# Performance work log

Measured on AMD Instinct MI355X. Metric: run time of the kernel, lower is better.

Reference implementation:

```python
import jax, jax.numpy as jnp
import numpy as np

NUM_USERS = 80000
NUM_ITEMS = 40000
NUM_NODES = NUM_USERS + NUM_ITEMS
LATENT_DIM = 64
N_LAYERS = 3
ALPHA = 0.8
E_POS = 3_000_000
E_NEG = 1_500_000
E_PATH = 2_000_000
N_PATHS = 6


def _make_edges(rng, n_edges, n_nodes):
    # sample keys, dedupe so COO is coalesced (distinct (row,col) pairs)
    keys = rng.integers(0, n_nodes * n_nodes, size=int(n_edges * 1.05), dtype=np.int64)
    keys = np.unique(keys)[:n_edges]
    assert keys.shape[0] == n_edges
    row = (keys // n_nodes).astype(np.int32)
    col = (keys % n_nodes).astype(np.int32)
    return row, col


def setup_inputs() -> dict:
    key = jax.random.key(0)
    k1, k2, k3, k4, k5 = jax.random.split(key, 5)
    rng = np.random.default_rng(0)

    pos_row, pos_col = _make_edges(rng, E_POS, NUM_NODES)
    neg_row, neg_col = _make_edges(rng, E_NEG, NUM_NODES)
    p_row, p_col = _make_edges(rng, E_PATH, NUM_NODES)

    # path membership counts: for each coalesced edge, how many times each of the
    # 6 path matrices contains it (0/1 here); at least one path per edge
    counts = (rng.random((E_PATH, N_PATHS)) < 0.5).astype(np.float32)
    empty = counts.sum(axis=1) == 0
    counts[empty, 0] = 1.0

    return {
        "user_emb": 0.1 * jax.random.normal(k1, (NUM_USERS, LATENT_DIM), jnp.float32),
        "item_emb": 0.1 * jax.random.normal(k2, (NUM_ITEMS, LATENT_DIM), jnp.float32),
        "theta": jnp.ones((N_PATHS,), jnp.float32) / N_PATHS,
        "pos_row": jnp.asarray(pos_row),
        "pos_col": jnp.asarray(pos_col),
        "pos_val": jax.random.uniform(k3, (E_POS,), jnp.float32, 0.01, 1.0),
        "neg_row": jnp.asarray(neg_row),
        "neg_col": jnp.asarray(neg_col),
        "neg_val": jax.random.uniform(k4, (E_NEG,), jnp.float32, 0.01, 1.0),
        "p_row": jnp.asarray(p_row),
        "p_col": jnp.asarray(p_col),
        "p_counts": jnp.asarray(counts),
    }


def _spmm(row, col, val, x, n_nodes):
    # y = A @ x with A given as COO edge list: gather + segment scatter-add
    return jax.ops.segment_sum(val[:, None] * x[col], row, num_segments=n_nodes)


def reference(user_emb, item_emb, theta, pos_row, pos_col, pos_val,
              neg_row, neg_col, neg_val, p_row, p_col, p_counts):
    n = NUM_NODES

    # ---- build path-weighted matrix (coalesce + sparse row softmax, eq.(2)) ----
    theta_w = jax.nn.softmax(theta)                 # [6]
    vals = p_counts @ theta_w                       # coalesced values per edge [E_path]
    exp_v = jnp.exp(vals)
    row_sums = jax.ops.segment_sum(exp_v, p_row, num_segments=n)
    soft_v = exp_v / (row_sums[p_row] + 1e-12)      # row-level sparse softmax

    # ---- PEE: E_0 = P @ all_emb ----
    all_emb = jnp.concatenate([user_emb, item_emb], axis=0)  # [N, D]
    e = _spmm(p_row, p_col, soft_v, all_emb, n)
    embs = [e]

    # ---- signed propagation ----
    for _ in range(N_LAYERS):
        e_pos = _spmm(pos_row, pos_col, pos_val, e, n)
        e_neg_a = _spmm(neg_row, neg_col, neg_val, e, n)
        e = e_pos + ALPHA * (e - e_neg_a)
        embs.append(e)

    light_out = jnp.mean(jnp.stack(embs, axis=1), axis=1)   # [N, D]
    users = light_out[:NUM_USERS]
    items = light_out[NUM_USERS:]
    return users, items
```

## Files before the change

### kernel.cpp

```cpp
#include <hip/hip_runtime.h>

#define NUM_USERS 80000
#define NUM_ITEMS 40000
#define NUM_NODES 120000
#define DIM 64
#define ALPHA_C 0.8f

typedef unsigned short u16;
typedef unsigned int u32;
typedef int   i2v __attribute__((ext_vector_type(2)));
typedef u32   u4v __attribute__((ext_vector_type(4)));
typedef float f4v __attribute__((ext_vector_type(4)));

__device__ __forceinline__ u16 f2bf(float f) {
    union { float f; u32 i; } v;
    v.f = f;
    u32 i = v.i;
    u32 r = (i + 0x7FFFu + ((i >> 16) & 1u)) >> 16;
    return (u16)r;
}
__device__ __forceinline__ float lo_bf(u32 u) { return __uint_as_float(u << 16); }
__device__ __forceinline__ float hi_bf(u32 u) { return __uint_as_float(u & 0xffff0000u); }

__device__ __forceinline__ void acc8(float* __restrict__ acc, float v, uint4 q) {
    const u32* p = (const u32*)&q;
#pragma unroll
    for (int k = 0; k < 4; ++k) {
        u32 u = p[k];
        acc[2 * k]     = fmaf(v, lo_bf(u), acc[2 * k]);
        acc[2 * k + 1] = fmaf(v, hi_bf(u), acc[2 * k + 1]);
    }
}

__device__ __forceinline__ uint4 ldrow(const u16* __restrict__ x, int c, int li) {
    return *((const uint4*)(x + (size_t)c * DIM) + li);
}

template <bool SUMV, bool PACKED>
__device__ __forceinline__ void seg_pipe(const int* __restrict__ cp0,
                                         const float* __restrict__ vp0,
                                         const i2v* __restrict__ ep0,
                                         int start, int end,
                                         const u16* __restrict__ x,
                                         int li,
                                         float* __restrict__ acc,
                                         float* __restrict__ vsum) {
    const int n = end - start;
    const int* cp = nullptr;
    const float* vp = nullptr;
    const i2v* ep = nullptr;
    if constexpr (PACKED) { ep = ep0 + start; }
    else { cp = cp0 + start; vp = vp0 + start; }

    auto LDE = [&](int i, int& c, float& v) {
        if constexpr (PACKED) {
            i2v e = ep[i];
            c = e.x;
            v = __int_as_float(e.y);
        } else {
            c = cp[i];
            v = vp[i];
        }
    };

    float s = 0.f;
    const int np = n >> 1;
    if (np >= 4) {
        int ca0, ca1, cb0, cb1, cc0, cc1, cd0, cd1;
        float va0, va1, vb0, vb1, vc0, vc1, vd0, vd1;
        LDE(0, ca0, va0); LDE(1, ca1, va1);
        LDE(2, cb0, vb0); LDE(3, cb1, vb1);
        LDE(4, cc0, vc0); LDE(5, cc1, vc1);
        LDE(6, cd0, vd0); LDE(7, cd1, vd1);
        uint4 xa0 = ldrow(x, ca0, li), xa1 = ldrow(x, ca1, li);
        uint4 xb0 = ldrow(x, cb0, li), xb1 = ldrow(x, cb1, li);
        for (int p = 4; p < np; ++p) {
            int ce0, ce1; float ve0, ve1;
            LDE(2 * p, ce0, ve0); LDE(2 * p + 1, ce1, ve1);
            uint4 xc0 = ldrow(x, cc0, li);
            uint4 xc1 = ldrow(x, cc1, li);
            acc8(acc, va0, xa0);
            acc8(acc, va1, xa1);
            if (SUMV) s += va0 + va1;
            va0 = vb0; va1 = vb1; vb0 = vc0; vb1 = vc1; vc0 = vd0; vc1 = vd1;
            vd0 = ve0; vd1 = ve1;
            cc0 = cd0; cc1 = cd1; cd0 = ce0; cd1 = ce1;
            xa0 = xb0; xa1 = xb1; xb0 = xc0; xb1 = xc1;
        }
        uint4 xc0 = ldrow(x, cc0, li), xc1 = ldrow(x, cc1, li);
        uint4 xd0 = ldrow(x, cd0, li), xd1 = ldrow(x, cd1, li);
        acc8(acc, va0, xa0); acc8(acc, va1, xa1);
        if (SUMV) s += va0 + va1;
        acc8(acc, vb0, xb0); acc8(acc, vb1, xb1);
        if (SUMV) s += vb0 + vb1;
        acc8(acc, vc0, xc0); acc8(acc, vc1, xc1);
        if (SUMV) s += vc0 + vc1;
        acc8(acc, vd0, xd0); acc8(acc, vd1, xd1);
        if (SUMV) s += vd0 + vd1;
        if (n & 1) {
            int c; float v;
            LDE(n - 1, c, v);
            uint4 xq = ldrow(x, c, li);
            acc8(acc, v, xq);
            if (SUMV) s += v;
        }
    } else {
        for (int e = 0; e < n; ++e) {
            int c; float v;
            LDE(e, c, v);
            uint4 xq = ldrow(x, c, li);
            acc8(acc, v, xq);
            if (SUMV) s += v;
        }
    }
    if (SUMV) *vsum = s;
}

__global__ void k_softmax_theta(const float* __restrict__ theta,
                                float* __restrict__ theta_w) {
    if (threadIdx.x == 0 && blockIdx.x == 0) {
        float m = -1e30f;
        for (int i = 0; i < 6; ++i) m = fmaxf(m, theta[i]);
        float e[6];
        float s = 0.f;
        for (int i = 0; i < 6; ++i) { e[i] = expf(theta[i] - m); s += e[i]; }
        for (int i = 0; i < 6; ++i) theta_w[i] = e[i] / s;
    }
}

__global__ void k_expv(const float* __restrict__ p_counts,
                       const float* __restrict__ theta_w,
                       float* __restrict__ exp_v, int E) {
    int i = blockIdx.x * blockDim.x + threadIdx.x;
    if (i >= E) return;
    const float* c = p_counts + (size_t)i * 6;
    float v = c[0] * theta_w[0] + c[1] * theta_w[1] + c[2] * theta_w[2] +
              c[3] * theta_w[3] + c[4] * theta_w[4] + c[5] * theta_w[5];
    exp_v[i] = expf(v);
}

__device__ __forceinline__ void lower_bound_ptr(const int* __restrict__ rows,
                                                int nnz, int r,
                                                int* __restrict__ ptr) {
    int lo = 0, hi = nnz;
    while (lo < hi) {
        int mid = (lo + hi) >> 1;
        if (rows[mid] < r) lo = mid + 1; else hi = mid;
    }
    ptr[r] = lo;
}

__global__ void k_row_ptr3(const int* __restrict__ rows_a, int nnz_a, int* __restrict__ pa,
                           const int* __restrict__ rows_b, int nnz_b, int* __restrict__ pb,
                           const int* __restrict__ rows_c, int nnz_c, int* __restrict__ pc) {
    int t = blockIdx.x * blockDim.x + threadIdx.x;
    int which = t / (NUM_NODES + 1);
    int r = t - which * (NUM_NODES + 1);
    if (which == 0) lower_bound_ptr(rows_a, nnz_a, r, pa);
    else if (which == 1) lower_bound_ptr(rows_b, nnz_b, r, pb);
    else if (which == 2) lower_bound_ptr(rows_c, nnz_c, r, pc);
}

__global__ void k_cvt(const float* __restrict__ user_emb,
                      const float* __restrict__ item_emb,
                      u16* __restrict__ emb16) {
    int i = blockIdx.x * blockDim.x + threadIdx.x;
    size_t f = (size_t)i * 4;
    const size_t UTOT = (size_t)NUM_USERS * DIM;
    const size_t TOT = (size_t)NUM_NODES * DIM;
    if (f >= TOT) return;
    float4 v = (f < UTOT) ? *(const float4*)(user_emb + f)
                          : *(const float4*)(item_emb + (f - UTOT));
    ushort4 o;
    o.x = f2bf(v.x); o.y = f2bf(v.y); o.z = f2bf(v.z); o.w = f2bf(v.w);
    *(ushort4*)(emb16 + f) = o;
}

__global__ void k_merge(const int* __restrict__ rp_p, const int* __restrict__ col_p,
                        const float* __restrict__ val_p,
                        const int* __restrict__ rp_n, const int* __restrict__ col_n,
                        const float* __restrict__ val_n,
                        i2v* __restrict__ mev, int* __restrict__ rp_m,
                        int nnz_total) {
    int t = blockIdx.x * blockDim.x + threadIdx.x;
    int row = t >> 3;
    if (row >= NUM_NODES) return;
    int li = threadIdx.x & 7;
    int sp = rp_p[row], np = rp_p[row + 1] - sp;
    int sn = rp_n[row], nn = rp_n[row + 1] - sn;
    int base = sp + sn;
    if (li == 0) {
        rp_m[row] = base;
        if (row == 0) rp_m[NUM_NODES] = nnz_total;
    }
    for (int i = li; i < np; i += 8) {
        i2v e;
        e.x = __builtin_nontemporal_load(col_p + sp + i);
        e.y = __float_as_int(__builtin_nontemporal_load(val_p + sp + i));
        __builtin_nontemporal_store(e, mev + base + i);
    }
    int b2 = base + np;
    for (int i = li; i < nn; i += 8) {
        i2v e;
        e.x = __builtin_nontemporal_load(col_n + sn + i);
        e.y = __float_as_int(-ALPHA_C * __builtin_nontemporal_load(val_n + sn + i));
        __builtin_nontemporal_store(e, mev + b2 + i);
    }
}

__global__ void k_path(const u16* __restrict__ emb16,
                       const float* __restrict__ exp_v,
                       const int* __restrict__ rp,
                       const int* __restrict__ cols,
                       u16* __restrict__ e0) {
    int t = blockIdx.x * blockDim.x + threadIdx.x;
    int row = t >> 3;
    if (row >= NUM_NODES) return;
    int li = threadIdx.x & 7;
    int start = rp[row], end = rp[row + 1];

    float acc[8];
#pragma unroll
    for (int k = 0; k < 8; ++k) acc[k] = 0.f;
    float s = 0.f;

    seg_pipe<true, false>(cols, exp_v, nullptr, start, end, emb16, li, acc, &s);

    float inv = 1.0f / (s + 1e-12f);
    u32 o[4];
#pragma unroll
    for (int k = 0; k < 4; ++k)
        o[k] = (u32)f2bf(acc[2 * k] * inv) | ((u32)f2bf(acc[2 * k + 1] * inv) << 16);
    u4v vv; vv.x = o[0]; vv.y = o[1]; vv.z = o[2]; vv.w = o[3];
    __builtin_nontemporal_store(vv, (u4v*)(e0 + (size_t)row * DIM) + li);
}

template <int FINAL>
__global__ void k_layer_t(const u16* __restrict__ e_in,
                          u16* __restrict__ e_out,
                          const u16* __restrict__ e0,
                          const u16* __restrict__ e1,
                          float* __restrict__ out,
                          const int* __restrict__ rp_m,
                          const i2v* __restrict__ mev) {
    int t = blockIdx.x * blockDim.x + threadIdx.x;
    int row = t >> 3;
    if (row >= NUM_NODES) return;
    int li = threadIdx.x & 7;

    float acc[8];
#pragma unroll
    for (int k = 0; k < 8; ++k) acc[k] = 0.f;

    seg_pipe<false, true>(nullptr, nullptr, mev, rp_m[row], rp_m[row + 1],
                          e_in, li, acc, nullptr);

    uint4 eq = *((const uint4*)(e_in + (size_t)row * DIM) + li);
    const u32* ep_ = (const u32*)&eq;
    float res[8];
#pragma unroll
    for (int k = 0; k < 4; ++k) {
        res[2 * k]     = acc[2 * k]     + ALPHA_C * lo_bf(ep_[k]);
        res[2 * k + 1] = acc[2 * k + 1] + ALPHA_C * hi_bf(ep_[k]);
    }

    if (FINAL) {
        u4v q0 = __builtin_nontemporal_load((const u4v*)(e0 + (size_t)row * DIM) + li);
        u4v q1 = __builtin_nontemporal_load((const u4v*)(e1 + (size_t)row * DIM) + li);
        float of[8];
#pragma unroll
        for (int k = 0; k < 4; ++k) {
            float lo = res[2 * k]     + lo_bf(ep_[k]) + lo_bf(q0[k]) + lo_bf(q1[k]);
            float hi = res[2 * k + 1] + hi_bf(ep_[k]) + hi_bf(q0[k]) + hi_bf(q1[k]);
            of[2 * k]     = 0.25f * lo;
            of[2 * k + 1] = 0.25f * hi;
        }
        f4v o0, o1;
        o0.x = of[0]; o0.y = of[1]; o0.z = of[2]; o0.w = of[3];
        o1.x = of[4]; o1.y = of[5]; o1.z = of[6]; o1.w = of[7];
        f4v* sp = (f4v*)(out + (size_t)row * DIM) + li * 2;
        __builtin_nontemporal_store(o0, sp);
        __builtin_nontemporal_store(o1, sp + 1);
    } else {
        u32 o[4];
#pragma unroll
        for (int k = 0; k < 4; ++k)
            o[k] = (u32)f2bf(res[2 * k]) | ((u32)f2bf(res[2 * k + 1]) << 16);
        u4v vv; vv.x = o[0]; vv.y = o[1]; vv.z = o[2]; vv.w = o[3];
        __builtin_nontemporal_store(vv, (u4v*)(e_out + (size_t)row * DIM) + li);
    }
}

extern "C" void kernel_launch(void* const* d_in, const int* in_sizes, int n_in,
                              void* d_out, int out_size, void* d_ws, size_t ws_size,
                              hipStream_t stream) {
    const float* user_emb = (const float*)d_in[0];
    const float* item_emb = (const float*)d_in[1];
    const float* theta    = (const float*)d_in[2];
    const int*   pos_row  = (const int*)d_in[3];
    const int*   pos_col  = (const int*)d_in[4];
    const float* pos_val  = (const float*)d_in[5];
    const int*   neg_row  = (const int*)d_in[6];
    const int*   neg_col  = (const int*)d_in[7];
    const float* neg_val  = (const float*)d_in[8];
    const int*   p_row    = (const int*)d_in[9];
    const int*   p_col    = (const int*)d_in[10];
    const float* p_counts = (const float*)d_in[11];
    const int E_pos  = in_sizes[3];
    const int E_neg  = in_sizes[6];
    const int E_path = in_sizes[9];

    char* wsb = (char*)d_ws;
    size_t off = 0;
    auto alloc = [&](size_t bytes) -> void* {
        void* p = wsb + off;
        off = (off + bytes + 255) & ~(size_t)255;
        return p;
    };
    float* theta_w = (float*)alloc(6 * sizeof(float));
    float* exp_v   = (float*)alloc((size_t)E_path * sizeof(float));
    int*   rp_pos  = (int*)alloc((size_t)(NUM_NODES + 1) * sizeof(int));
    int*   rp_neg  = (int*)alloc((size_t)(NUM_NODES + 1) * sizeof(int));
    int*   rp_path = (int*)alloc((size_t)(NUM_NODES + 1) * sizeof(int));
    int*   rp_m    = (int*)alloc((size_t)(NUM_NODES + 1) * sizeof(int));
    i2v*   mev     = (i2v*)alloc((size_t)(E_pos + E_neg) * sizeof(i2v));
    u16*   emb16   = (u16*)alloc((size_t)NUM_NODES * DIM * sizeof(u16));
    u16*   e0      = (u16*)alloc((size_t)NUM_NODES * DIM * sizeof(u16));
    u16*   e1      = (u16*)alloc((size_t)NUM_NODES * DIM * sizeof(u16));
    u16*   e2      = emb16;
    float* outp    = (float*)d_out;

    k_softmax_theta<<<1, 64, 0, stream>>>(theta, theta_w);
    k_expv<<<(E_path + 255) / 256, 256, 0, stream>>>(p_counts, theta_w, exp_v, E_path);

    int total_rp = 3 * (NUM_NODES + 1);
    k_row_ptr3<<<(total_rp + 255) / 256, 256, 0, stream>>>(
        pos_row, E_pos, rp_pos, neg_row, E_neg, rp_neg, p_row, E_path, rp_path);

    int cvt_threads = (NUM_NODES * DIM) / 4;
    k_cvt<<<(cvt_threads + 255) / 256, 256, 0, stream>>>(user_emb, item_emb, emb16);

    int row_blocks = (NUM_NODES + 31) / 32;

    k_merge<<<row_blocks, 256, 0, stream>>>(rp_pos, pos_col, pos_val,
                                            rp_neg, neg_col, neg_val,
                                            mev, rp_m, E_pos + E_neg);

    k_path<<<row_blocks, 256, 0, stream>>>(emb16, exp_v, rp_path, p_col, e0);
    k_layer_t<0><<<row_blocks, 256, 0, stream>>>(e0, e1, nullptr, nullptr, nullptr,
                                                 rp_m, mev);
    k_layer_t<0><<<row_blocks, 256, 0, stream>>>(e1, e2, nullptr, nullptr, nullptr,
                                                 rp_m, mev);
    k_layer_t<1><<<row_blocks, 256, 0, stream>>>(e2, nullptr, e0, e1, outp,
                                                 rp_m, mev);
}
```

Measured before the change: 492.8 us.

## Fuse theta softmax into expv, pack path edges, merge signed edges per-edge

Folds the theta softmax into the exp-value kernel, which now also packs the path column and exp value into one interleaved array, so the path SpMM reads a single stream. The per-row merge of positive and negative edges becomes a per-edge scatter that uses row pointers, and the merged row pointer is computed in the row-pointer kernel. Edge reads switch to nontemporal loads. Embedding outputs switch to normal stores so the next layer can hit in cache. Each thread now recomputes the six-way softmax, and an extra pass of binary searches is added for the merged pointer.

After: 563.5 us. 14.3% more time.

```diff
diff --git a/kernel.cpp b/kernel.cpp
--- a/kernel.cpp
+++ b/kernel.cpp
@@ -36,79 +36,75 @@
     return *((const uint4*)(x + (size_t)c * DIM) + li);
 }
 
-template <bool SUMV, bool PACKED>
-__device__ __forceinline__ void seg_pipe(const int* __restrict__ cp0,
-                                         const float* __restrict__ vp0,
-                                         const i2v* __restrict__ ep0,
+__device__ __forceinline__ i2v ntl_e(const i2v* __restrict__ p) {
+    return __builtin_nontemporal_load(p);
+}
+
+template <bool SUMV>
+__device__ __forceinline__ void seg_pipe(const i2v* __restrict__ ep0,
                                          int start, int end,
                                          const u16* __restrict__ x,
                                          int li,
                                          float* __restrict__ acc,
                                          float* __restrict__ vsum) {
     const int n = end - start;
-    const int* cp = nullptr;
-    const float* vp = nullptr;
-    const i2v* ep = nullptr;
-    if constexpr (PACKED) { ep = ep0 + start; }
-    else { cp = cp0 + start; vp = vp0 + start; }
-
-    auto LDE = [&](int i, int& c, float& v) {
-        if constexpr (PACKED) {
-            i2v e = ep[i];
-            c = e.x;
-            v = __int_as_float(e.y);
-        } else {
-            c = cp[i];
-            v = vp[i];
-        }
-    };
-
+    const i2v* ep = ep0 + start;
     float s = 0.f;
     const int np = n >> 1;
     if (np >= 4) {
-        int ca0, ca1, cb0, cb1, cc0, cc1, cd0, cd1;
-        float va0, va1, vb0, vb1, vc0, vc1, vd0, vd1;
-        LDE(0, ca0, va0); LDE(1, ca1, va1);
-        LDE(2, cb0, vb0); LDE(3, cb1, vb1);
-        LDE(4, cc0, vc0); LDE(5, cc1, vc1);
-        LDE(6, cd0, vd0); LDE(7, cd1, vd1);
-        uint4 xa0 = ldrow(x, ca0, li), xa1 = ldrow(x, ca1, li);
-        uint4 xb0 = ldrow(x, cb0, li), xb1 = ldrow(x, cb1, li);
+        i2v ea0 = ntl_e(ep + 0), ea1 = ntl_e(ep + 1);
+        i2v eb0 = ntl_e(ep + 2), eb1 = ntl_e(ep + 3);
+        i2v ec0 = ntl_e(ep + 4), ec1 = ntl_e(ep + 5);
+        i2v ed0 = ntl_e(ep + 6), ed1 = ntl_e(ep + 7);
+        uint4 xa0 = ldrow(x, ea0.x, li), xa1 = ldrow(x, ea1.x, li);
+        uint4 xb0 = ldrow(x, eb0.x, li), xb1 = ldrow(x, eb1.x, li);
         for (int p = 4; p < np; ++p) {
-            int ce0, ce1; float ve0, ve1;
-            LDE(2 * p, ce0, ve0); LDE(2 * p + 1, ce1, ve1);
-            uint4 xc0 = ldrow(x, cc0, li);
-            uint4 xc1 = ldrow(x, cc1, li);
+            i2v ee0 = ntl_e(ep + 2 * p);
+            i2v ee1 = ntl_e(ep + 2 * p + 1);
+            uint4 xc0 = ldrow(x, ec0.x, li);
+            uint4 xc1 = ldrow(x, ec1.x, li);
+            float va0 = __int_as_float(ea0.y), va1 = __int_as_float(ea1.y);
             acc8(acc, va0, xa0);
             acc8(acc, va1, xa1);
             if (SUMV) s += va0 + va1;
-            va0 = vb0; va1 = vb1; vb0 = vc0; vb1 = vc1; vc0 = vd0; vc1 = vd1;
-            vd0 = ve0; vd1 = ve1;
-            cc0 = cd0; cc1 = cd1; cd0 = ce0; cd1 = ce1;
+            ea0 = eb0; ea1 = eb1; eb0 = ec0; eb1 = ec1;
+            ec0 = ed0; ec1 = ed1; ed0 = ee0; ed1 = ee1;
             xa0 = xb0; xa1 = xb1; xb0 = xc0; xb1 = xc1;
         }
-        uint4 xc0 = ldrow(x, cc0, li), xc1 = ldrow(x, cc1, li);
-        uint4 xd0 = ldrow(x, cd0, li), xd1 = ldrow(x, cd1, li);
-        acc8(acc, va0, xa0); acc8(acc, va1, xa1);
-        if (SUMV) s += va0 + va1;
-        acc8(acc, vb0, xb0); acc8(acc, vb1, xb1);
-        if (SUMV) s += vb0 + vb1;
-        acc8(acc, vc0, xc0); acc8(acc, vc1, xc1);
-        if (SUMV) s += vc0 + vc1;
-        acc8(acc, vd0, xd0); acc8(acc, vd1, xd1);
-        if (SUMV) s += vd0 + vd1;
+        uint4 xc0 = ldrow(x, ec0.x, li), xc1 = ldrow(x, ec1.x, li);
+        uint4 xd0 = ldrow(x, ed0.x, li), xd1 = ldrow(x, ed1.x, li);
+        {
+            float va0 = __int_as_float(ea0.y), va1 = __int_as_float(ea1.y);
+            acc8(acc, va0, xa0); acc8(acc, va1, xa1);
+            if (SUMV) s += va0 + va1;
+        }
+        {
+            float vb0 = __int_as_float(eb0.y), vb1 = __int_as_float(eb1.y);
+            acc8(acc, vb0, xb0); acc8(acc, vb1, xb1);
+            if (SUMV) s += vb0 + vb1;
+        }
+        {
+            float vc0 = __int_as_float(ec0.y), vc1 = __int_as_float(ec1.y);
+            acc8(acc, vc0, xc0); acc8(acc, vc1, xc1);
+            if (SUMV) s += vc0 + vc1;
+        }
+        {
+            float vd0 = __int_as_float(ed0.y), vd1 = __int_as_float(ed1.y);
+            acc8(acc, vd0, xd0); acc8(acc, vd1, xd1);
+            if (SUMV) s += vd0 + vd1;
+        }
         if (n & 1) {
-            int c; float v;
-            LDE(n - 1, c, v);
-            uint4 xq = ldrow(x, c, li);
+            i2v eq = ntl_e(ep + n - 1);
+            float v = __int_as_float(eq.y);
+            uint4 xq = ldrow(x, eq.x, li);
             acc8(acc, v, xq);
             if (SUMV) s += v;
         }
     } else {
         for (int e = 0; e < n; ++e) {
-            int c; float v;
-            LDE(e, c, v);
-            uint4 xq = ldrow(x, c, li);
+            i2v eq = ntl_e(ep + e);
+            float v = __int_as_float(eq.y);
+            uint4 xq = ldrow(x, eq.x, li);
             acc8(acc, v, xq);
             if (SUMV) s += v;
         }
@@ -116,49 +112,50 @@
     if (SUMV) *vsum = s;
 }
 
-__global__ void k_softmax_theta(const float* __restrict__ theta,
-                                float* __restrict__ theta_w) {
-    if (threadIdx.x == 0 && blockIdx.x == 0) {
-        float m = -1e30f;
-        for (int i = 0; i < 6; ++i) m = fmaxf(m, theta[i]);
-        float e[6];
-        float s = 0.f;
-        for (int i = 0; i < 6; ++i) { e[i] = expf(theta[i] - m); s += e[i]; }
-        for (int i = 0; i < 6; ++i) theta_w[i] = e[i] / s;
-    }
-}
-
-__global__ void k_expv(const float* __restrict__ p_counts,
-                       const float* __restrict__ theta_w,
-                       float* __restrict__ exp_v, int E) {
+__global__ void k_expv_pack(const float* __restrict__ p_counts,
+                            const float* __restrict__ theta,
+                            const int* __restrict__ p_col,
+                            i2v* __restrict__ pev, int E) {
     int i = blockIdx.x * blockDim.x + threadIdx.x;
     if (i >= E) return;
+    float m = -1e30f;
+    for (int k = 0; k < 6; ++k) m = fmaxf(m, theta[k]);
+    float e[6];
+    float s = 0.f;
+    for (int k = 0; k < 6; ++k) { e[k] = expf(theta[k] - m); s += e[k]; }
+    float w0 = e[0] / s, w1 = e[1] / s, w2 = e[2] / s,
+          w3 = e[3] / s, w4 = e[4] / s, w5 = e[5] / s;
     const float* c = p_counts + (size_t)i * 6;
-    float v = c[0] * theta_w[0] + c[1] * theta_w[1] + c[2] * theta_w[2] +
-              c[3] * theta_w[3] + c[4] * theta_w[4] + c[5] * theta_w[5];
-    exp_v[i] = expf(v);
-}
-
-__device__ __forceinline__ void lower_bound_ptr(const int* __restrict__ rows,
-                                                int nnz, int r,
-                                                int* __restrict__ ptr) {
+    float v = c[0] * w0 + c[1] * w1 + c[2] * w2 +
+              c[3] * w3 + c[4] * w4 + c[5] * w5;
+    i2v o;
+    o.x = __builtin_nontemporal_load(p_col + i);
+    o.y = __float_as_int(expf(v));
+    __builtin_nontemporal_store(o, pev + i);
+}
+
+__device__ __forceinline__ int lower_bound_v(const int* __restrict__ rows,
+                                             int nnz, int r) {
     int lo = 0, hi = nnz;
     while (lo < hi) {
         int mid = (lo + hi) >> 1;
         if (rows[mid] < r) lo = mid + 1; else hi = mid;
     }
-    ptr[r] = lo;
-}
-
-__global__ void k_row_ptr3(const int* __restrict__ rows_a, int nnz_a, int* __restrict__ pa,
+    return lo;
+}
+
+__global__ void k_row_ptr4(const int* __restrict__ rows_a, int nnz_a, int* __restrict__ pa,
                            const int* __restrict__ rows_b, int nnz_b, int* __restrict__ pb,
-                           const int* __restrict__ rows_c, int nnz_c, int* __restrict__ pc) {
+                           const int* __restrict__ rows_c, int nnz_c, int* __restrict__ pc,
+                           int* __restrict__ pm) {
     int t = blockIdx.x * blockDim.x + threadIdx.x;
     int which = t / (NUM_NODES + 1);
     int r = t - which * (NUM_NODES + 1);
-    if (which == 0) lower_bound_ptr(rows_a, nnz_a, r, pa);
-    else if (which == 1) lower_bound_ptr(rows_b, nnz_b, r, pb);
-    else if (which == 2) lower_bound_ptr(rows_c, nnz_c, r, pc);
+    if (which == 0) pa[r] = lower_bound_v(rows_a, nnz_a, r);
+    else if (which == 1) pb[r] = lower_bound_v(rows_b, nnz_b, r);
+    else if (which == 2) pc[r] = lower_bound_v(rows_c, nnz_c, r);
+    else if (which == 3) pm[r] = lower_bound_v(rows_a, nnz_a, r) +
+                                 lower_bound_v(rows_b, nnz_b, r);
 }
 
 __global__ void k_cvt(const float* __restrict__ user_emb,
@@ -169,49 +166,40 @@
     const size_t UTOT = (size_t)NUM_USERS * DIM;
     const size_t TOT = (size_t)NUM_NODES * DIM;
     if (f >= TOT) return;
-    float4 v = (f < UTOT) ? *(const float4*)(user_emb + f)
-                          : *(const float4*)(item_emb + (f - UTOT));
+    f4v v = (f < UTOT) ? __builtin_nontemporal_load((const f4v*)(user_emb + f))
+                       : __builtin_nontemporal_load((const f4v*)(item_emb + (f - UTOT)));
     ushort4 o;
     o.x = f2bf(v.x); o.y = f2bf(v.y); o.z = f2bf(v.z); o.w = f2bf(v.w);
     *(ushort4*)(emb16 + f) = o;
 }
 
-__global__ void k_merge(const int* __restrict__ rp_p, const int* __restrict__ col_p,
-                        const float* __restrict__ val_p,
-                        const int* __restrict__ rp_n, const int* __restrict__ col_n,
-                        const float* __restrict__ val_n,
-                        i2v* __restrict__ mev, int* __restrict__ rp_m,
-                        int nnz_total) {
-    int t = blockIdx.x * blockDim.x + threadIdx.x;
-    int row = t >> 3;
-    if (row >= NUM_NODES) return;
-    int li = threadIdx.x & 7;
-    int sp = rp_p[row], np = rp_p[row + 1] - sp;
-    int sn = rp_n[row], nn = rp_n[row + 1] - sn;
-    int base = sp + sn;
-    if (li == 0) {
-        rp_m[row] = base;
-        if (row == 0) rp_m[NUM_NODES] = nnz_total;
-    }
-    for (int i = li; i < np; i += 8) {
+__global__ void k_merge_e(const int* __restrict__ row_p, const int* __restrict__ col_p,
+                          const float* __restrict__ val_p,
+                          const int* __restrict__ row_n, const int* __restrict__ col_n,
+                          const float* __restrict__ val_n,
+                          const int* __restrict__ rp_p, const int* __restrict__ rp_n,
+                          i2v* __restrict__ mev, int E_pos, int E_tot) {
+    int g = blockIdx.x * blockDim.x + threadIdx.x;
+    if (g >= E_tot) return;
+    if (g < E_pos) {
+        int r = __builtin_nontemporal_load(row_p + g);
         i2v e;
-        e.x = __builtin_nontemporal_load(col_p + sp + i);
-        e.y = __float_as_int(__builtin_nontemporal_load(val_p + sp + i));
-        __builtin_nontemporal_store(e, mev + base + i);
-    }
-    int b2 = base + np;
-    for (int i = li; i < nn; i += 8) {
+        e.x = __builtin_nontemporal_load(col_p + g);
+        e.y = __float_as_int(__builtin_nontemporal_load(val_p + g));
+        __builtin_nontemporal_store(e, mev + (size_t)g + rp_n[r]);
+    } else {
+        int i = g - E_pos;
+        int r = __builtin_nontemporal_load(row_n + i);
         i2v e;
-        e.x = __builtin_nontemporal_load(col_n + sn + i);
-        e.y = __float_as_int(-ALPHA_C * __builtin_nontemporal_load(val_n + sn + i));
-        __builtin_nontemporal_store(e, mev + b2 + i);
+        e.x = __builtin_nontemporal_load(col_n + i);
+        e.y = __float_as_int(-ALPHA_C * __builtin_nontemporal_load(val_n + i));
+        __builtin_nontemporal_store(e, mev + (size_t)i + rp_p[r + 1]);
     }
 }
 
 __global__ void k_path(const u16* __restrict__ emb16,
-                       const float* __restrict__ exp_v,
+                       const i2v* __restrict__ pev,
                        const int* __restrict__ rp,
-                       const int* __restrict__ cols,
                        u16* __restrict__ e0) {
     int t = blockIdx.x * blockDim.x + threadIdx.x;
     int row = t >> 3;
@@ -224,15 +212,14 @@
     for (int k = 0; k < 8; ++k) acc[k] = 0.f;
     float s = 0.f;
 
-    seg_pipe<true, false>(cols, exp_v, nullptr, start, end, emb16, li, acc, &s);
+    seg_pipe<true>(pev, start, end, emb16, li, acc, &s);
 
     float inv = 1.0f / (s + 1e-12f);
     u32 o[4];
 #pragma unroll
     for (int k = 0; k < 4; ++k)
         o[k] = (u32)f2bf(acc[2 * k] * inv) | ((u32)f2bf(acc[2 * k + 1] * inv) << 16);
-    u4v vv; vv.x = o[0]; vv.y = o[1]; vv.z = o[2]; vv.w = o[3];
-    __builtin_nontemporal_store(vv, (u4v*)(e0 + (size_t)row * DIM) + li);
+    *((uint4*)(e0 + (size_t)row * DIM) + li) = *(uint4*)o;
 }
 
 template <int FINAL>
@@ -248,14 +235,14 @@
     if (row >= NUM_NODES) return;
     int li = threadIdx.x & 7;
 
+    uint4 eq = *((const uint4*)(e_in + (size_t)row * DIM) + li);
+
     float acc[8];
 #pragma unroll
     for (int k = 0; k < 8; ++k) acc[k] = 0.f;
 
-    seg_pipe<false, true>(nullptr, nullptr, mev, rp_m[row], rp_m[row + 1],
-                          e_in, li, acc, nullptr);
-
-    uint4 eq = *((const uint4*)(e_in + (size_t)row * DIM) + li);
+    seg_pipe<false>(mev, rp_m[row], rp_m[row + 1], e_in, li, acc, nullptr);
+
     const u32* ep_ = (const u32*)&eq;
     float res[8];
 #pragma unroll
@@ -286,8 +273,7 @@
 #pragma unroll
         for (int k = 0; k < 4; ++k)
             o[k] = (u32)f2bf(res[2 * k]) | ((u32)f2bf(res[2 * k + 1]) << 16);
-        u4v vv; vv.x = o[0]; vv.y = o[1]; vv.z = o[2]; vv.w = o[3];
-        __builtin_nontemporal_store(vv, (u4v*)(e_out + (size_t)row * DIM) + li);
+        *((uint4*)(e_out + (size_t)row * DIM) + li) = *(uint4*)o;
     }
 }
 
@@ -317,8 +303,7 @@
         off = (off + bytes + 255) & ~(size_t)255;
         return p;
     };
-    float* theta_w = (float*)alloc(6 * sizeof(float));
-    float* exp_v   = (float*)alloc((size_t)E_path * sizeof(float));
+    i2v*   pev     = (i2v*)alloc((size_t)E_path * sizeof(i2v));
     int*   rp_pos  = (int*)alloc((size_t)(NUM_NODES + 1) * sizeof(int));
     int*   rp_neg  = (int*)alloc((size_t)(NUM_NODES + 1) * sizeof(int));
     int*   rp_path = (int*)alloc((size_t)(NUM_NODES + 1) * sizeof(int));
@@ -330,23 +315,25 @@
     u16*   e2      = emb16;
     float* outp    = (float*)d_out;
 
-    k_softmax_theta<<<1, 64, 0, stream>>>(theta, theta_w);
-    k_expv<<<(E_path + 255) / 256, 256, 0, stream>>>(p_counts, theta_w, exp_v, E_path);
-
-    int total_rp = 3 * (NUM_NODES + 1);
-    k_row_ptr3<<<(total_rp + 255) / 256, 256, 0, stream>>>(
-        pos_row, E_pos, rp_pos, neg_row, E_neg, rp_neg, p_row, E_path, rp_path);
+    k_expv_pack<<<(E_path + 255) / 256, 256, 0, stream>>>(p_counts, theta, p_col,
+                                                          pev, E_path);
+
+    int total_rp = 4 * (NUM_NODES + 1);
+    k_row_ptr4<<<(total_rp + 255) / 256, 256, 0, stream>>>(
+        pos_row, E_pos, rp_pos, neg_row, E_neg, rp_neg, p_row, E_path, rp_path,
+        rp_m);
 
     int cvt_threads = (NUM_NODES * DIM) / 4;
     k_cvt<<<(cvt_threads + 255) / 256, 256, 0, stream>>>(user_emb, item_emb, emb16);
 
+    int E_tot = E_pos + E_neg;
+    k_merge_e<<<(E_tot + 255) / 256, 256, 0, stream>>>(
+        pos_row, pos_col, pos_val, neg_row, neg_col, neg_val,
+        rp_pos, rp_neg, mev, E_pos, E_tot);
+
     int row_blocks = (NUM_NODES + 31) / 32;
 
-    k_merge<<<row_blocks, 256, 0, stream>>>(rp_pos, pos_col, pos_val,
-                                            rp_neg, neg_col, neg_val,
-                                            mev, rp_m, E_pos + E_neg);
-
-    k_path<<<row_blocks, 256, 0, stream>>>(emb16, exp_v, rp_path, p_col, e0);
+    k_path<<<row_blocks, 256, 0, stream>>>(emb16, pev, rp_path, e0);
     k_layer_t<0><<<row_blocks, 256, 0, stream>>>(e0, e1, nullptr, nullptr, nullptr,
                                                  rp_m, mev);
     k_layer_t<0><<<row_blocks, 256, 0, stream>>>(e1, e2, nullptr, nullptr, nullptr,
```
